# Kernel optimization log

Hardware: AMD Instinct MI355X
Metric: run time of the kernel (lower is better)

Reference implementation:

```python
import jax, jax.numpy as jnp
import numpy as np


def setup_inputs() -> dict:
    key = jax.random.key(0)
    k1, k2 = jax.random.split(key)
    B, T, D = 16, 1024, 256
    z = jax.random.normal(k1, (B, T, D), dtype=jnp.float32)
    gt_dT = jax.random.normal(k2, (B, T, T, 4), dtype=jnp.float32)
    sigma = jnp.full((4,), 0.1, dtype=jnp.float32)
    return {"z": z, "gt_dT": gt_dT, "sigma": sigma}


def reference(z, gt_dT, sigma):
    # z: [B,T,D], gt_dT: [B,T,T,4], sigma: [4]
    B, T, D = z.shape
    # Gaussian kernel over pairwise displacements -> w: [B,T,T]
    inv2s2 = 1.0 / (2.0 * sigma * sigma)  # [4]
    kernel = jnp.einsum('btsk,k->bts', gt_dT * gt_dT, inv2s2)
    w = jnp.exp(-kernel)  # [B,T,T]

    z2 = jnp.sum(z * z, axis=-1)          # [B,T]
    w_col_sum = jnp.sum(w, axis=2)        # [B,T]
    term1 = jnp.sum(z2 * w_col_sum, axis=1)  # [B]

    wz = jnp.einsum('bts,bsd->btd', w, z)    # [B,T,D]
    term2 = jnp.sum(wz * z, axis=(1, 2))     # [B]

    w_row_sum = jnp.sum(w, axis=1)           # [B,T]
    term3 = jnp.sum(z2 * w_row_sum, axis=1)  # [B]

    loss = jnp.mean(term1 - 2.0 * term2 + term3) / (T * T)
    return loss
```

## Files before the change

### kernel.cpp

```cpp
#include <hip/hip_runtime.h>
#include <hip/hip_bf16.h>
#include <stdint.h>

#define BB 16
#define TT 1024
#define DD 256
#define NACC 64

typedef __attribute__((ext_vector_type(8))) short short8;
typedef __attribute__((ext_vector_type(4))) float floatx4;
typedef __attribute__((ext_vector_type(4))) float fvec4;

__device__ __forceinline__ unsigned short f2bf(float f) {
    union { float f; unsigned int u; } c; c.f = f;
    unsigned int u = c.u;
    unsigned int r = (u + 0x7FFFu + ((u >> 16) & 1u)) >> 16;
    return (unsigned short)r;
}

__global__ __launch_bounds__(256) void prep_kernel(
    const float* __restrict__ z, float* __restrict__ z2,
    unsigned short* __restrict__ zb, double* __restrict__ acc) {
    if (blockIdx.x == 0 && threadIdx.x < NACC) acc[threadIdx.x] = 0.0;
    const int lane = threadIdx.x & 63;
    const int row  = blockIdx.x * 4 + (threadIdx.x >> 6);
    const float4 v = ((const float4*)(z + (size_t)row * DD))[lane];
    float ss = v.x * v.x + v.y * v.y + v.z * v.z + v.w * v.w;
    ushort4 o;
    o.x = f2bf(v.x); o.y = f2bf(v.y); o.z = f2bf(v.z); o.w = f2bf(v.w);
    ((ushort4*)(zb + (size_t)row * DD))[lane] = o;
#pragma unroll
    for (int off = 32; off > 0; off >>= 1) ss += __shfl_down(ss, off);
    if (lane == 0) z2[row] = ss;
}

__global__ __launch_bounds__(256) void patch_kernel(
    const unsigned short* __restrict__ zb, const float* __restrict__ z2,
    const float* __restrict__ gt, const float* __restrict__ sigma,
    double* __restrict__ acc) {
    const float LOG2E = 1.4426950408889634f;
    const float s0v = sigma[0], s1v = sigma[1], s2v = sigma[2], s3v = sigma[3];
    const float nc0 = -LOG2E * 0.5f / (s0v * s0v);
    const float nc1 = -LOG2E * 0.5f / (s1v * s1v);
    const float nc2 = -LOG2E * 0.5f / (s2v * s2v);
    const float nc3 = -LOG2E * 0.5f / (s3v * s3v);

    const int tid  = threadIdx.x;
    const int lane = tid & 63;
    const int quad = lane >> 4;
    const int m    = lane & 15;
    const int wid  = blockIdx.x * 4 + (tid >> 6);

    const int b   = wid >> 10;
    const int rem = wid & 1023;
    const int t0  = (rem >> 5) << 5;
    const int s0  = (rem & 31) << 5;

    const float* gtb = gt + (size_t)b * TT * TT * 4;
    const int    tq  = t0 + quad * 4;

    fvec4 gtv[8];
#pragma unroll
    for (int r = 0; r < 2; ++r) {
        const size_t row0 = (size_t)(tq + r) * TT;
        const size_t row1 = (size_t)(tq + 16 + r) * TT;
        gtv[r * 4 + 0] = __builtin_nontemporal_load((const fvec4*)(gtb + (row0 + (s0 + m)) * 4));
        gtv[r * 4 + 1] = __builtin_nontemporal_load((const fvec4*)(gtb + (row0 + (s0 + 16 + m)) * 4));
        gtv[r * 4 + 2] = __builtin_nontemporal_load((const fvec4*)(gtb + (row1 + (s0 + m)) * 4));
        gtv[r * 4 + 3] = __builtin_nontemporal_load((const fvec4*)(gtb + (row1 + (s0 + 16 + m)) * 4));
    }

    const unsigned short* zrow = zb + (size_t)b * TT * DD;
    const short8* at0 = (const short8*)(zrow + (t0 + m) * DD + quad * 8);
    const short8* at1 = (const short8*)(zrow + (t0 + 16 + m) * DD + quad * 8);
    const short8* bs0 = (const short8*)(zrow + (s0 + m) * DD + quad * 8);
    const short8* bs1 = (const short8*)(zrow + (s0 + 16 + m) * DD + quad * 8);

    floatx4 g00 = {0.f, 0.f, 0.f, 0.f};
    floatx4 g01 = {0.f, 0.f, 0.f, 0.f};
    floatx4 g10 = {0.f, 0.f, 0.f, 0.f};
    floatx4 g11 = {0.f, 0.f, 0.f, 0.f};
#pragma unroll
    for (int k = 0; k < 8; ++k) {
        const short8 a0 = at0[k * 4];
        const short8 a1 = at1[k * 4];
        const short8 b0 = bs0[k * 4];
        const short8 b1 = bs1[k * 4];
        g00 = __builtin_amdgcn_mfma_f32_16x16x32_bf16(a0, b0, g00, 0, 0, 0);
        g01 = __builtin_amdgcn_mfma_f32_16x16x32_bf16(a0, b1, g01, 0, 0, 0);
        g10 = __builtin_amdgcn_mfma_f32_16x16x32_bf16(a1, b0, g10, 0, 0, 0);
        g11 = __builtin_amdgcn_mfma_f32_16x16x32_bf16(a1, b1, g11, 0, 0, 0);
    }

    const float* z2b  = z2 + b * TT;
    const float  z2s0 = z2b[s0 + m];
    const float  z2s1 = z2b[s0 + 16 + m];

    float partial = 0.f;

#pragma unroll
    for (int half = 0; half < 2; ++half) {
        if (half == 1) {
#pragma unroll
            for (int r = 0; r < 2; ++r) {
                const size_t row0 = (size_t)(tq + 2 + r) * TT;
                const size_t row1 = (size_t)(tq + 18 + r) * TT;
                gtv[r * 4 + 0] = __builtin_nontemporal_load((const fvec4*)(gtb + (row0 + (s0 + m)) * 4));
                gtv[r * 4 + 1] = __builtin_nontemporal_load((const fvec4*)(gtb + (row0 + (s0 + 16 + m)) * 4));
                gtv[r * 4 + 2] = __builtin_nontemporal_load((const fvec4*)(gtb + (row1 + (s0 + m)) * 4));
                gtv[r * 4 + 3] = __builtin_nontemporal_load((const fvec4*)(gtb + (row1 + (s0 + 16 + m)) * 4));
            }
        }
#pragma unroll
        for (int r = 0; r < 2; ++r) {
            const int rr = half * 2 + r;
            const float z2t0 = z2b[tq + rr];
            const float z2t1 = z2b[tq + 16 + rr];
            const float e00 = z2t0 + z2s0, e01 = z2t0 + z2s1;
            const float e10 = z2t1 + z2s0, e11 = z2t1 + z2s1;
            {
                const fvec4 d = gtv[r * 4 + 0];
                const float k2 = fmaf(nc3, d.w * d.w, fmaf(nc2, d.z * d.z,
                                 fmaf(nc1, d.y * d.y, nc0 * d.x * d.x)));
                partial = fmaf(exp2f(k2), fmaf(-2.f, g00[rr], e00), partial);
            }
            {
                const fvec4 d = gtv[r * 4 + 1];
                const float k2 = fmaf(nc3, d.w * d.w, fmaf(nc2, d.z * d.z,
                                 fmaf(nc1, d.y * d.y, nc0 * d.x * d.x)));
                partial = fmaf(exp2f(k2), fmaf(-2.f, g01[rr], e01), partial);
            }
            {
                const fvec4 d = gtv[r * 4 + 2];
                const float k2 = fmaf(nc3, d.w * d.w, fmaf(nc2, d.z * d.z,
                                 fmaf(nc1, d.y * d.y, nc0 * d.x * d.x)));
                partial = fmaf(exp2f(k2), fmaf(-2.f, g10[rr], e10), partial);
            }
            {
                const fvec4 d = gtv[r * 4 + 3];
                const float k2 = fmaf(nc3, d.w * d.w, fmaf(nc2, d.z * d.z,
                                 fmaf(nc1, d.y * d.y, nc0 * d.x * d.x)));
                partial = fmaf(exp2f(k2), fmaf(-2.f, g11[rr], e11), partial);
            }
        }
    }

#pragma unroll
    for (int off = 32; off > 0; off >>= 1) partial += __shfl_down(partial, off);
    __shared__ float red[4];
    if (lane == 0) red[tid >> 6] = partial;
    __syncthreads();
    if (tid == 0)
        atomicAdd(&acc[blockIdx.x & (NACC - 1)],
                  (double)(red[0] + red[1] + red[2] + red[3]));
}

__global__ void finalize_kernel(const double* __restrict__ acc, float* __restrict__ out) {
    double v = acc[threadIdx.x];
#pragma unroll
    for (int off = 32; off > 0; off >>= 1) v += __shfl_down(v, off);
    if (threadIdx.x == 0)
        out[0] = (float)(v * (1.0 / ((double)BB * (double)TT * (double)TT)));
}

extern "C" void kernel_launch(void* const* d_in, const int* in_sizes, int n_in,
                              void* d_out, int out_size, void* d_ws, size_t ws_size,
                              hipStream_t stream) {
    const float* z     = (const float*)d_in[0];
    const float* gt    = (const float*)d_in[1];
    const float* sigma = (const float*)d_in[2];
    float* out = (float*)d_out;

    char* ws = (char*)d_ws;
    double* acc        = (double*)ws;
    float* z2          = (float*)(ws + 512);
    unsigned short* zb = (unsigned short*)(ws + 512 + (size_t)BB * TT * sizeof(float));

    prep_kernel<<<BB * TT / 4, 256, 0, stream>>>(z, z2, zb, acc);
    patch_kernel<<<BB * (TT / 32) * (TT / 32) / 4, 256, 0, stream>>>(zb, z2, gt, sigma, acc);
    finalize_kernel<<<1, 64, 0, stream>>>(acc, out);
}
```

Baseline: 385.9 us.

## Prefetch second half of gt via async global-to-LDS loads and fuse finalize

The second half of each wave's gt tile is now issued at kernel start as direct global-to-LDS loads, replacing the register loads that were issued after the MFMA phase. This puts all gt traffic in flight before the matrix work, so memory latency overlaps with compute without raising register pressure. The block reduction through shared memory becomes one double atomic per wave. The separate finalize kernel is replaced by a last-block ticket scheme inside the patch kernel, removing one launch at the cost of an extra atomic and fences per block.

```diff
diff --git a/kernel.cpp b/kernel.cpp
--- a/kernel.cpp
+++ b/kernel.cpp
@@ -1,5 +1,4 @@
 #include <hip/hip_runtime.h>
-#include <hip/hip_bf16.h>
 #include <stdint.h>
 
 #define BB 16
@@ -10,6 +9,11 @@
 typedef __attribute__((ext_vector_type(8))) short short8;
 typedef __attribute__((ext_vector_type(4))) float floatx4;
 typedef __attribute__((ext_vector_type(4))) float fvec4;
+
+#define GLDS16(gp, lp)                                                              \
+    __builtin_amdgcn_global_load_lds(                                               \
+        (__attribute__((address_space(1))) const void*)(gp),                        \
+        (__attribute__((address_space(3))) void*)(lp), 16, 0, 0)
 
 __device__ __forceinline__ unsigned short f2bf(float f) {
     union { float f; unsigned int u; } c; c.f = f;
@@ -20,8 +24,12 @@
 
 __global__ __launch_bounds__(256) void prep_kernel(
     const float* __restrict__ z, float* __restrict__ z2,
-    unsigned short* __restrict__ zb, double* __restrict__ acc) {
-    if (blockIdx.x == 0 && threadIdx.x < NACC) acc[threadIdx.x] = 0.0;
+    unsigned short* __restrict__ zb, double* __restrict__ acc,
+    unsigned int* __restrict__ ticket) {
+    if (blockIdx.x == 0) {
+        if (threadIdx.x < NACC) acc[threadIdx.x] = 0.0;
+        if (threadIdx.x == NACC) *ticket = 0u;
+    }
     const int lane = threadIdx.x & 63;
     const int row  = blockIdx.x * 4 + (threadIdx.x >> 6);
     const float4 v = ((const float4*)(z + (size_t)row * DD))[lane];
@@ -37,7 +45,10 @@
 __global__ __launch_bounds__(256) void patch_kernel(
     const unsigned short* __restrict__ zb, const float* __restrict__ z2,
     const float* __restrict__ gt, const float* __restrict__ sigma,
-    double* __restrict__ acc) {
+    double* __restrict__ acc, unsigned int* __restrict__ ticket,
+    float* __restrict__ out) {
+    __shared__ __attribute__((aligned(16))) float lds_gt[4][8][64][4];
+
     const float LOG2E = 1.4426950408889634f;
     const float s0v = sigma[0], s1v = sigma[1], s2v = sigma[2], s3v = sigma[3];
     const float nc0 = -LOG2E * 0.5f / (s0v * s0v);
@@ -47,9 +58,10 @@
 
     const int tid  = threadIdx.x;
     const int lane = tid & 63;
+    const int wv   = tid >> 6;
     const int quad = lane >> 4;
     const int m    = lane & 15;
-    const int wid  = blockIdx.x * 4 + (tid >> 6);
+    const int wid  = blockIdx.x * 4 + wv;
 
     const int b   = wid >> 10;
     const int rem = wid & 1023;
@@ -68,6 +80,16 @@
         gtv[r * 4 + 1] = __builtin_nontemporal_load((const fvec4*)(gtb + (row0 + (s0 + 16 + m)) * 4));
         gtv[r * 4 + 2] = __builtin_nontemporal_load((const fvec4*)(gtb + (row1 + (s0 + m)) * 4));
         gtv[r * 4 + 3] = __builtin_nontemporal_load((const fvec4*)(gtb + (row1 + (s0 + 16 + m)) * 4));
+    }
+
+#pragma unroll
+    for (int r = 0; r < 2; ++r) {
+        const size_t row0 = (size_t)(tq + 2 + r) * TT;
+        const size_t row1 = (size_t)(tq + 18 + r) * TT;
+        GLDS16(gtb + (row0 + (s0 + m)) * 4,      &lds_gt[wv][r * 4 + 0][0][0]);
+        GLDS16(gtb + (row0 + (s0 + 16 + m)) * 4, &lds_gt[wv][r * 4 + 1][0][0]);
+        GLDS16(gtb + (row1 + (s0 + m)) * 4,      &lds_gt[wv][r * 4 + 2][0][0]);
+        GLDS16(gtb + (row1 + (s0 + 16 + m)) * 4, &lds_gt[wv][r * 4 + 3][0][0]);
     }
 
     const unsigned short* zrow = zb + (size_t)b * TT * DD;
@@ -99,68 +121,93 @@
     float partial = 0.f;
 
 #pragma unroll
-    for (int half = 0; half < 2; ++half) {
-        if (half == 1) {
-#pragma unroll
-            for (int r = 0; r < 2; ++r) {
-                const size_t row0 = (size_t)(tq + 2 + r) * TT;
-                const size_t row1 = (size_t)(tq + 18 + r) * TT;
-                gtv[r * 4 + 0] = __builtin_nontemporal_load((const fvec4*)(gtb + (row0 + (s0 + m)) * 4));
-                gtv[r * 4 + 1] = __builtin_nontemporal_load((const fvec4*)(gtb + (row0 + (s0 + 16 + m)) * 4));
-                gtv[r * 4 + 2] = __builtin_nontemporal_load((const fvec4*)(gtb + (row1 + (s0 + m)) * 4));
-                gtv[r * 4 + 3] = __builtin_nontemporal_load((const fvec4*)(gtb + (row1 + (s0 + 16 + m)) * 4));
-            }
-        }
-#pragma unroll
-        for (int r = 0; r < 2; ++r) {
-            const int rr = half * 2 + r;
-            const float z2t0 = z2b[tq + rr];
-            const float z2t1 = z2b[tq + 16 + rr];
-            const float e00 = z2t0 + z2s0, e01 = z2t0 + z2s1;
-            const float e10 = z2t1 + z2s0, e11 = z2t1 + z2s1;
-            {
-                const fvec4 d = gtv[r * 4 + 0];
-                const float k2 = fmaf(nc3, d.w * d.w, fmaf(nc2, d.z * d.z,
-                                 fmaf(nc1, d.y * d.y, nc0 * d.x * d.x)));
-                partial = fmaf(exp2f(k2), fmaf(-2.f, g00[rr], e00), partial);
-            }
-            {
-                const fvec4 d = gtv[r * 4 + 1];
-                const float k2 = fmaf(nc3, d.w * d.w, fmaf(nc2, d.z * d.z,
-                                 fmaf(nc1, d.y * d.y, nc0 * d.x * d.x)));
-                partial = fmaf(exp2f(k2), fmaf(-2.f, g01[rr], e01), partial);
-            }
-            {
-                const fvec4 d = gtv[r * 4 + 2];
-                const float k2 = fmaf(nc3, d.w * d.w, fmaf(nc2, d.z * d.z,
-                                 fmaf(nc1, d.y * d.y, nc0 * d.x * d.x)));
-                partial = fmaf(exp2f(k2), fmaf(-2.f, g10[rr], e10), partial);
-            }
-            {
-                const fvec4 d = gtv[r * 4 + 3];
-                const float k2 = fmaf(nc3, d.w * d.w, fmaf(nc2, d.z * d.z,
-                                 fmaf(nc1, d.y * d.y, nc0 * d.x * d.x)));
-                partial = fmaf(exp2f(k2), fmaf(-2.f, g11[rr], e11), partial);
-            }
+    for (int r = 0; r < 2; ++r) {
+        const float z2t0 = z2b[tq + r];
+        const float z2t1 = z2b[tq + 16 + r];
+        const float e00 = z2t0 + z2s0, e01 = z2t0 + z2s1;
+        const float e10 = z2t1 + z2s0, e11 = z2t1 + z2s1;
+        {
+            const fvec4 d = gtv[r * 4 + 0];
+            const float k2 = fmaf(nc3, d.w * d.w, fmaf(nc2, d.z * d.z,
+                             fmaf(nc1, d.y * d.y, nc0 * d.x * d.x)));
+            partial = fmaf(exp2f(k2), fmaf(-2.f, g00[r], e00), partial);
+        }
+        {
+            const fvec4 d = gtv[r * 4 + 1];
+            const float k2 = fmaf(nc3, d.w * d.w, fmaf(nc2, d.z * d.z,
+                             fmaf(nc1, d.y * d.y, nc0 * d.x * d.x)));
+            partial = fmaf(exp2f(k2), fmaf(-2.f, g01[r], e01), partial);
+        }
+        {
+            const fvec4 d = gtv[r * 4 + 2];
+            const float k2 = fmaf(nc3, d.w * d.w, fmaf(nc2, d.z * d.z,
+                             fmaf(nc1, d.y * d.y, nc0 * d.x * d.x)));
+            partial = fmaf(exp2f(k2), fmaf(-2.f, g10[r], e10), partial);
+        }
+        {
+            const fvec4 d = gtv[r * 4 + 3];
+            const float k2 = fmaf(nc3, d.w * d.w, fmaf(nc2, d.z * d.z,
+                             fmaf(nc1, d.y * d.y, nc0 * d.x * d.x)));
+            partial = fmaf(exp2f(k2), fmaf(-2.f, g11[r], e11), partial);
+        }
+    }
+
+    asm volatile("s_waitcnt vmcnt(0)" ::: "memory");
+#pragma unroll
+    for (int r = 0; r < 2; ++r) {
+        const int rr = 2 + r;
+        const float z2t0 = z2b[tq + rr];
+        const float z2t1 = z2b[tq + 16 + rr];
+        const float e00 = z2t0 + z2s0, e01 = z2t0 + z2s1;
+        const float e10 = z2t1 + z2s0, e11 = z2t1 + z2s1;
+        const fvec4 d0 = *(const fvec4*)&lds_gt[wv][r * 4 + 0][lane][0];
+        const fvec4 d1 = *(const fvec4*)&lds_gt[wv][r * 4 + 1][lane][0];
+        const fvec4 d2 = *(const fvec4*)&lds_gt[wv][r * 4 + 2][lane][0];
+        const fvec4 d3 = *(const fvec4*)&lds_gt[wv][r * 4 + 3][lane][0];
+        {
+            const float k2 = fmaf(nc3, d0.w * d0.w, fmaf(nc2, d0.z * d0.z,
+                             fmaf(nc1, d0.y * d0.y, nc0 * d0.x * d0.x)));
+            partial = fmaf(exp2f(k2), fmaf(-2.f, g00[rr], e00), partial);
+        }
+        {
+            const float k2 = fmaf(nc3, d1.w * d1.w, fmaf(nc2, d1.z * d1.z,
+                             fmaf(nc1, d1.y * d1.y, nc0 * d1.x * d1.x)));
+            partial = fmaf(exp2f(k2), fmaf(-2.f, g01[rr], e01), partial);
+        }
+        {
+            const float k2 = fmaf(nc3, d2.w * d2.w, fmaf(nc2, d2.z * d2.z,
+                             fmaf(nc1, d2.y * d2.y, nc0 * d2.x * d2.x)));
+            partial = fmaf(exp2f(k2), fmaf(-2.f, g10[rr], e10), partial);
+        }
+        {
+            const float k2 = fmaf(nc3, d3.w * d3.w, fmaf(nc2, d3.z * d3.z,
+                             fmaf(nc1, d3.y * d3.y, nc0 * d3.x * d3.x)));
+            partial = fmaf(exp2f(k2), fmaf(-2.f, g11[rr], e11), partial);
         }
     }
 
 #pragma unroll
     for (int off = 32; off > 0; off >>= 1) partial += __shfl_down(partial, off);
-    __shared__ float red[4];
-    if (lane == 0) red[tid >> 6] = partial;
+    if (lane == 0) atomicAdd(&acc[wid & (NACC - 1)], (double)partial);
+
     __syncthreads();
-    if (tid == 0)
-        atomicAdd(&acc[blockIdx.x & (NACC - 1)],
-                  (double)(red[0] + red[1] + red[2] + red[3]));
-}
-
-__global__ void finalize_kernel(const double* __restrict__ acc, float* __restrict__ out) {
-    double v = acc[threadIdx.x];
-#pragma unroll
-    for (int off = 32; off > 0; off >>= 1) v += __shfl_down(v, off);
-    if (threadIdx.x == 0)
-        out[0] = (float)(v * (1.0 / ((double)BB * (double)TT * (double)TT)));
+    if (wv == 0) {
+        unsigned int t = 0;
+        if (lane == 0) {
+            __threadfence();
+            t = atomicAdd(ticket, 1u);
+        }
+        t = __shfl(t, 0);
+        if (t == gridDim.x - 1) {
+            __threadfence();
+            double v = __hip_atomic_load(&acc[lane], __ATOMIC_RELAXED,
+                                         __HIP_MEMORY_SCOPE_AGENT);
+#pragma unroll
+            for (int off = 32; off > 0; off >>= 1) v += __shfl_down(v, off);
+            if (lane == 0)
+                out[0] = (float)(v * (1.0 / ((double)BB * (double)TT * (double)TT)));
+        }
+    }
 }
 
 extern "C" void kernel_launch(void* const* d_in, const int* in_sizes, int n_in,
@@ -172,11 +219,12 @@
     float* out = (float*)d_out;
 
     char* ws = (char*)d_ws;
-    double* acc        = (double*)ws;
-    float* z2          = (float*)(ws + 512);
-    unsigned short* zb = (unsigned short*)(ws + 512 + (size_t)BB * TT * sizeof(float));
-
-    prep_kernel<<<BB * TT / 4, 256, 0, stream>>>(z, z2, zb, acc);
-    patch_kernel<<<BB * (TT / 32) * (TT / 32) / 4, 256, 0, stream>>>(zb, z2, gt, sigma, acc);
-    finalize_kernel<<<1, 64, 0, stream>>>(acc, out);
-}
+    double* acc          = (double*)ws;
+    unsigned int* ticket = (unsigned int*)(ws + 512);
+    float* z2            = (float*)(ws + 1024);
+    unsigned short* zb   = (unsigned short*)(ws + 1024 + (size_t)BB * TT * sizeof(float));
+
+    prep_kernel<<<BB * TT / 4, 256, 0, stream>>>(z, z2, zb, acc, ticket);
+    patch_kernel<<<BB * (TT / 32) * (TT / 32) / 4, 256, 0, stream>>>(
+        zb, z2, gt, sigma, acc, ticket, out);
+}
```

Result: slower. 575.4 us (+49.1%).
